# Kernel optimization log

Hardware: AMD Instinct MI355X
Metric: run time of the kernel (lower is better)

The kernel has to match this reference:

```python
import jax, jax.numpy as jnp
import numpy as np

B, N, M = 16384, 2048, 2048


def setup_inputs() -> dict:
    key = jax.random.key(0)
    k1, k2 = jax.random.split(key, 2)
    X = jax.random.normal(k1, (B, N), dtype=jnp.float32)
    # master weights, kaiming-ish small scale
    W = jax.random.normal(k2, (M, N), dtype=jnp.float32) * 0.02
    bias = jnp.zeros((M,), dtype=jnp.float32)
    return {"X": X, "W": W, "bias": bias}


def reference(X, W, bias):
    # AbsMax ternary quantization: scale = max|W|, W_q = round(W/scale) clamped to {-1,0,1}
    scale = jnp.max(jnp.abs(W))
    W_ternary = jnp.clip(jnp.round(W / (scale + 1e-8)), -1.0, 1.0)
    # Y = X @ (W_ternary * scale)^T + bias   (the int32 bit-packing in the torch
    # code is computed but ignored by the dense F.linear, so it does not affect output)
    Y = X @ (W_ternary * scale).T + bias
    return Y
```

## Files before the change

### kernel.cpp

```cpp
#include <hip/hip_runtime.h>
#include <stdint.h>

typedef unsigned int uint32;

#define N_DIM 2048
#define M_DIM 2048
#define ROWS_PER_BLOCK 8
#define CAP 79
#define SLOTS 80


__global__ void k_init(uint32* scale_bits) {
    if (threadIdx.x == 0) *scale_bits = 0u;
}

__global__ __launch_bounds__(256) void k_absmax(const float* __restrict__ W,
                                                uint32* __restrict__ scale_bits) {
    int tid = blockIdx.x * 256 + threadIdx.x;
    int stride = gridDim.x * 256;
    const float4* W4 = (const float4*)W;
    const int total4 = (M_DIM * N_DIM) / 4;
    float mx = 0.f;
    for (int i = tid; i < total4; i += stride) {
        float4 v = W4[i];
        mx = fmaxf(mx, fmaxf(fmaxf(fabsf(v.x), fabsf(v.y)),
                             fmaxf(fabsf(v.z), fabsf(v.w))));
    }
    for (int off = 32; off > 0; off >>= 1)
        mx = fmaxf(mx, __shfl_down(mx, off));
    if ((threadIdx.x & 63) == 0)
        atomicMax(scale_bits, __float_as_uint(mx));
}

__global__ __launch_bounds__(256) void k_quant(const float* __restrict__ W,
                                               const uint32* __restrict__ scale_bits,
                                               int* __restrict__ nnz,
                                               uint32* __restrict__ entries) {
    const int m    = (blockIdx.x * 256 + threadIdx.x) >> 6;
    const int lane = threadIdx.x & 63;
    const float s  = __uint_as_float(*scale_bits) + 1e-8f;
    const float lo = 0.4999995f * s;
    const float hi = 0.5000005f * s;
    const float4* Wr4 = (const float4*)(W + (size_t)m * N_DIM);
    const unsigned long long lmask = (1ull << lane) - 1ull;
    int cnt = 0;
#pragma unroll
    for (int it = 0; it < N_DIM / 4 / 64; ++it) {
        const float4 v = Wr4[it * 64 + lane];
        const float w[4] = {v.x, v.y, v.z, v.w};
#pragma unroll
        for (int j = 0; j < 4; ++j) {
            const float a = fabsf(w[j]);
            bool nzf;
            if (a < lo)      nzf = false;
            else if (a > hi) nzf = true;
            else             nzf = (rintf(w[j] / s) != 0.f);
            const unsigned long long mask = __ballot(nzf);
            if (nzf) {
                const int slot = cnt + __popcll(mask & lmask);
                if (slot < CAP) {
                    const uint32 n = (uint32)((it * 64 + lane) * 4 + j);
                    entries[slot * M_DIM + m] = (n << 1) | (w[j] < 0.f ? 1u : 0u);
                }
            }
            cnt += __popcll(mask);
        }
    }
    if (lane == 0) nnz[m] = cnt < CAP ? cnt : CAP;
}

__device__ __forceinline__ uint32 f2bf_rne(float f) {
    uint32 b = __float_as_uint(f);
    return (b + 0x7fffu + ((b >> 16) & 1u)) >> 16;
}

__global__ __launch_bounds__(512) void k_gemm(const float* __restrict__ X,
                                              const float* __restrict__ bias,
                                              const uint32* __restrict__ scale_bits,
                                              const int* __restrict__ nnz,
                                              const uint32* __restrict__ entries,
                                              float* __restrict__ Y) {
    __shared__ __align__(16) uint32 xs[N_DIM * 4];
    const int t = threadIdx.x;
    const int r0 = blockIdx.x * ROWS_PER_BLOCK;

    {
        const int u = t & 3;
        const int q = t >> 2;
        const float4* Xa = (const float4*)(X + (size_t)(r0 + 2 * u) * N_DIM);
        const float4* Xb = (const float4*)(X + (size_t)(r0 + 2 * u + 1) * N_DIM);
#pragma unroll
        for (int k = 0; k < 4; ++k) {
            const int c4 = q + (k << 7);
            const float4 va = Xa[c4];
            const float4 vb = Xb[c4];
            const float wa[4] = {va.x, va.y, va.z, va.w};
            const float wb[4] = {vb.x, vb.y, vb.z, vb.w};
#pragma unroll
            for (int i = 0; i < 4; ++i) {
                const uint32 packed = f2bf_rne(wa[i]) | (f2bf_rne(wb[i]) << 16);
                const int idx = (c4 << 4) + (i << 2) + u;
                xs[idx ^ (((idx >> 5) & 7) << 2)] = packed;
            }
        }
    }
    __syncthreads();

    const float scale = __uint_as_float(*scale_bits);
#pragma unroll 1
    for (int j = 0; j < 4; ++j) {
        const int m = t + (j << 9);
        const int nz = nnz[m];
        float a0 = 0.f, a1 = 0.f, a2 = 0.f, a3 = 0.f;
        float a4 = 0.f, a5 = 0.f, a6 = 0.f, a7 = 0.f;
        uint32 e = entries[m];
        for (int s = 0; s < nz; ++s) {
            const uint32 en = entries[(size_t)(s + 1) * M_DIM + m];
            const int n = (int)(e >> 1);
            const float sg = (e & 1u) ? -1.f : 1.f;
            const int base = n << 2;
            const int addr = base ^ (((base >> 5) & 7) << 2);
            const uint4 w = *(const uint4*)(xs + addr);
            a0 = fmaf(sg, __uint_as_float(w.x << 16),          a0);
            a1 = fmaf(sg, __uint_as_float(w.x & 0xffff0000u),  a1);
            a2 = fmaf(sg, __uint_as_float(w.y << 16),          a2);
            a3 = fmaf(sg, __uint_as_float(w.y & 0xffff0000u),  a3);
            a4 = fmaf(sg, __uint_as_float(w.z << 16),          a4);
            a5 = fmaf(sg, __uint_as_float(w.z & 0xffff0000u),  a5);
            a6 = fmaf(sg, __uint_as_float(w.w << 16),          a6);
            a7 = fmaf(sg, __uint_as_float(w.w & 0xffff0000u),  a7);
            e = en;
        }
        const float b = bias[m];
        float* Yp = Y + (size_t)r0 * M_DIM + m;
        Yp[0 * M_DIM] = fmaf(scale, a0, b);
        Yp[1 * M_DIM] = fmaf(scale, a1, b);
        Yp[2 * M_DIM] = fmaf(scale, a2, b);
        Yp[3 * M_DIM] = fmaf(scale, a3, b);
        Yp[4 * M_DIM] = fmaf(scale, a4, b);
        Yp[5 * M_DIM] = fmaf(scale, a5, b);
        Yp[6 * M_DIM] = fmaf(scale, a6, b);
        Yp[7 * M_DIM] = fmaf(scale, a7, b);
    }
}

extern "C" void kernel_launch(void* const* d_in, const int* in_sizes, int n_in,
                              void* d_out, int out_size, void* d_ws, size_t ws_size,
                              hipStream_t stream) {
    const float* X    = (const float*)d_in[0];
    const float* W    = (const float*)d_in[1];
    const float* bias = (const float*)d_in[2];
    float* Y = (float*)d_out;

    uint32* scale_bits = (uint32*)d_ws;
    int*    nnz        = (int*)d_ws + 1024;
    uint32* entries    = (uint32*)d_ws + 1024 + M_DIM;

    const int B = in_sizes[0] / N_DIM;

    hipLaunchKernelGGL(k_init,   dim3(1),                  dim3(64),  0, stream, scale_bits);
    hipLaunchKernelGGL(k_absmax, dim3(512),                dim3(256), 0, stream, W, scale_bits);
    hipLaunchKernelGGL(k_quant,  dim3(M_DIM * 64 / 256),   dim3(256), 0, stream, W, scale_bits, nnz, entries);
    hipLaunchKernelGGL(k_gemm,   dim3(B / ROWS_PER_BLOCK), dim3(512), 0, stream,
                       X, bias, scale_bits, nnz, entries, Y);
}
```

Baseline: 333.3 us.

## Precompute swizzled LDS addresses in sparse entries and make GEMM loop wave-uniform

The quantizer now stores pre-swizzled LDS byte offsets with the sign bit in the sparse entry list. It pads unused slots with an entry that points at a zeroed LDS word, so the GEMM loop can run a wave-uniform trip count (wave max of nnz) with no per-lane bounds. The inner loop software-pipelines the next LDS load and derives the sign with bit ops instead of a select, which cuts VALU address math and divergent loop control. The absmax kernel also reduces within the block before doing one atomic per block, and uses half as many blocks. Padded lanes do wasted FMAs on zeros, and the quant kernel performs extra stores.

Result: faster. 292.5 us (-12.3%).

```diff
diff --git a/kernel.cpp b/kernel.cpp
--- a/kernel.cpp
+++ b/kernel.cpp
@@ -8,6 +8,7 @@
 #define ROWS_PER_BLOCK 8
 #define CAP 79
 #define SLOTS 80
+#define ZERO_ENTRY 32768u
 
 
 __global__ void k_init(uint32* scale_bits) {
@@ -16,6 +17,7 @@
 
 __global__ __launch_bounds__(256) void k_absmax(const float* __restrict__ W,
                                                 uint32* __restrict__ scale_bits) {
+    __shared__ float red[4];
     int tid = blockIdx.x * 256 + threadIdx.x;
     int stride = gridDim.x * 256;
     const float4* W4 = (const float4*)W;
@@ -28,8 +30,12 @@
     }
     for (int off = 32; off > 0; off >>= 1)
         mx = fmaxf(mx, __shfl_down(mx, off));
-    if ((threadIdx.x & 63) == 0)
+    if ((threadIdx.x & 63) == 0) red[threadIdx.x >> 6] = mx;
+    __syncthreads();
+    if (threadIdx.x == 0) {
+        mx = fmaxf(fmaxf(red[0], red[1]), fmaxf(red[2], red[3]));
         atomicMax(scale_bits, __float_as_uint(mx));
+    }
 }
 
 __global__ __launch_bounds__(256) void k_quant(const float* __restrict__ W,
@@ -60,13 +66,18 @@
                 const int slot = cnt + __popcll(mask & lmask);
                 if (slot < CAP) {
                     const uint32 n = (uint32)((it * 64 + lane) * 4 + j);
-                    entries[slot * M_DIM + m] = (n << 1) | (w[j] < 0.f ? 1u : 0u);
+                    const uint32 base  = n << 2;
+                    const uint32 addrw = base ^ (((base >> 5) & 7) << 2);
+                    entries[slot * M_DIM + m] = (addrw << 2) | (w[j] < 0.f ? 1u : 0u);
                 }
             }
             cnt += __popcll(mask);
         }
     }
-    if (lane == 0) nnz[m] = cnt < CAP ? cnt : CAP;
+    const int c = cnt < CAP ? cnt : CAP;
+    for (int s2 = c + lane; s2 < SLOTS; s2 += 64)
+        entries[(size_t)s2 * M_DIM + m] = ZERO_ENTRY;
+    if (lane == 0) nnz[m] = c;
 }
 
 __device__ __forceinline__ uint32 f2bf_rne(float f) {
@@ -80,7 +91,7 @@
                                               const int* __restrict__ nnz,
                                               const uint32* __restrict__ entries,
                                               float* __restrict__ Y) {
-    __shared__ __align__(16) uint32 xs[N_DIM * 4];
+    __shared__ __align__(16) uint32 xs[N_DIM * 4 + 4];
     const int t = threadIdx.x;
     const int r0 = blockIdx.x * ROWS_PER_BLOCK;
 
@@ -104,23 +115,29 @@
             }
         }
     }
+    if (t < 4) xs[N_DIM * 4 + t] = 0u;
     __syncthreads();
 
     const float scale = __uint_as_float(*scale_bits);
 #pragma unroll 1
     for (int j = 0; j < 4; ++j) {
         const int m = t + (j << 9);
-        const int nz = nnz[m];
+        int wm = nnz[m];
+#pragma unroll
+        for (int off = 32; off > 0; off >>= 1)
+            wm = max(wm, __shfl_xor(wm, off));
+        const int wmax = __builtin_amdgcn_readfirstlane(wm);
+
         float a0 = 0.f, a1 = 0.f, a2 = 0.f, a3 = 0.f;
         float a4 = 0.f, a5 = 0.f, a6 = 0.f, a7 = 0.f;
-        uint32 e = entries[m];
-        for (int s = 0; s < nz; ++s) {
-            const uint32 en = entries[(size_t)(s + 1) * M_DIM + m];
-            const int n = (int)(e >> 1);
-            const float sg = (e & 1u) ? -1.f : 1.f;
-            const int base = n << 2;
-            const int addr = base ^ (((base >> 5) & 7) << 2);
-            const uint4 w = *(const uint4*)(xs + addr);
+        const uint32* ep = entries + m;
+        uint32 e = ep[0];
+        uint4 w = *(const uint4*)((const char*)xs + (e & 0xFFFFFFF0u));
+        float sg = __uint_as_float(0x3f800000u | (e << 31));
+        for (int s = 0; s < wmax; ++s) {
+            const uint32 en = ep[(size_t)(s + 1) * M_DIM];
+            const uint4 wn = *(const uint4*)((const char*)xs + (en & 0xFFFFFFF0u));
+            const float sgn = __uint_as_float(0x3f800000u | (en << 31));
             a0 = fmaf(sg, __uint_as_float(w.x << 16),          a0);
             a1 = fmaf(sg, __uint_as_float(w.x & 0xffff0000u),  a1);
             a2 = fmaf(sg, __uint_as_float(w.y << 16),          a2);
@@ -129,7 +146,8 @@
             a5 = fmaf(sg, __uint_as_float(w.z & 0xffff0000u),  a5);
             a6 = fmaf(sg, __uint_as_float(w.w << 16),          a6);
             a7 = fmaf(sg, __uint_as_float(w.w & 0xffff0000u),  a7);
-            e = en;
+            w = wn;
+            sg = sgn;
         }
         const float b = bias[m];
         float* Yp = Y + (size_t)r0 * M_DIM + m;
@@ -159,7 +177,7 @@
     const int B = in_sizes[0] / N_DIM;
 
     hipLaunchKernelGGL(k_init,   dim3(1),                  dim3(64),  0, stream, scale_bits);
-    hipLaunchKernelGGL(k_absmax, dim3(512),                dim3(256), 0, stream, W, scale_bits);
+    hipLaunchKernelGGL(k_absmax, dim3(256),                dim3(256), 0, stream, W, scale_bits);
     hipLaunchKernelGGL(k_quant,  dim3(M_DIM * 64 / 256),   dim3(256), 0, stream, W, scale_bits, nnz, entries);
     hipLaunchKernelGGL(k_gemm,   dim3(B / ROWS_PER_BLOCK), dim3(512), 0, stream,
                        X, bias, scale_bits, nnz, entries, Y);
```
